# Kernel tuning notes

Measured on AMD Instinct MI355X. Metric: run time of the kernel, lower is better.

Reference implementation:

```python
import jax, jax.numpy as jnp
import numpy as np

EMB = 1024
HEADS = 16
HEAD_DIM = EMB // HEADS
DFF = 4 * EMB
EPS = 1e-5


def setup_inputs() -> dict:
    key = jax.random.key(0)
    ks = jax.random.split(key, 16)
    s = 0.02
    return {
        "x": jax.random.normal(ks[0], (4, 2048, EMB), dtype=jnp.float32),
        "Wq_w": jax.random.normal(ks[1], (EMB, EMB), jnp.float32) * s,
        "Wq_b": jnp.zeros((EMB,), jnp.float32),
        "Wk_w": jax.random.normal(ks[2], (EMB, EMB), jnp.float32) * s,
        "Wk_b": jnp.zeros((EMB,), jnp.float32),
        "Wv_w": jax.random.normal(ks[3], (EMB, EMB), jnp.float32) * s,
        "Wv_b": jnp.zeros((EMB,), jnp.float32),
        "Wo_w": jax.random.normal(ks[4], (EMB, EMB), jnp.float32) * s,
        "Wo_b": jnp.zeros((EMB,), jnp.float32),
        "l1_w": jax.random.normal(ks[5], (DFF, EMB), jnp.float32) * s,
        "l1_b": jnp.zeros((DFF,), jnp.float32),
        "l2_w": jax.random.normal(ks[6], (EMB, DFF), jnp.float32) * s,
        "l2_b": jnp.zeros((EMB,), jnp.float32),
        "n1_scale": jnp.ones((EMB,), jnp.float32),
        "n1_shift": jnp.zeros((EMB,), jnp.float32),
        "n2_scale": jnp.ones((EMB,), jnp.float32),
        "n2_shift": jnp.zeros((EMB,), jnp.float32),
    }


def _layernorm(x, scale, shift):
    # Faithful to the source: mean over last dim, but var over the WHOLE
    # tensor (torch.var with no dim), and divides by var (not std), eps added after.
    mean = jnp.mean(x, axis=-1, keepdims=True)
    var = jnp.var(x)  # scalar, correction=0
    x_norm = (x - mean) / var + EPS
    return x_norm * scale + shift


def _block_forward(x, Wq_w, Wq_b, Wk_w, Wk_b, Wv_w, Wv_b, Wo_w, Wo_b,
                   l1_w, l1_b, l2_w, l2_b, n1_scale, n1_shift, n2_scale, n2_shift):
    B, T, C = x.shape
    shortcut = x
    h = _layernorm(x, n1_scale, n1_shift)

    def proj(w, b):
        y = jnp.einsum('btc,oc->bto', h, w) + b
        return y.reshape(B, T, HEADS, HEAD_DIM).transpose(0, 2, 1, 3)  # bhtd

    q = proj(Wq_w, Wq_b)
    k = proj(Wk_w, Wk_b)
    v = proj(Wv_w, Wv_b)

    scores = jnp.einsum('bhtd,bhsd->bhts', q, k)
    causal = jnp.triu(jnp.ones((T, T), dtype=bool), 1)
    scores = jnp.where(causal, -jnp.inf, scores)
    weights = jax.nn.softmax(scores / jnp.sqrt(jnp.float32(HEAD_DIM)), axis=-1)
    ctx = jnp.einsum('bhts,bhsd->bhtd', weights, v)
    ctx = ctx.transpose(0, 2, 1, 3).reshape(B, T, C)
    attn_out = jnp.einsum('btc,oc->bto', ctx, Wo_w) + Wo_b

    x = attn_out + shortcut
    shortcut = x
    h = _layernorm(x, n2_scale, n2_shift)
    h = jnp.einsum('btc,fc->btf', h, l1_w) + l1_b
    h = jax.nn.gelu(h, approximate=False)
    h = jnp.einsum('btf,cf->btc', h, l2_w) + l2_b
    return h + shortcut


def reference(x, Wq_w, Wq_b, Wk_w, Wk_b, Wv_w, Wv_b, Wo_w, Wo_b,
              l1_w, l1_b, l2_w, l2_b, n1_scale, n1_shift, n2_scale, n2_shift):
    return _block_forward(x, Wq_w, Wq_b, Wk_w, Wk_b, Wv_w, Wv_b, Wo_w, Wo_b,
                          l1_w, l1_b, l2_w, l2_b, n1_scale, n1_shift, n2_scale, n2_shift)
```

## Files before the change

### kernel.cpp

```cpp
#include <hip/hip_runtime.h>
#include <cstdint>

#define EMB   1024
#define HEADS 16
#define HDIM  64
#define DFF   4096
#define TLEN  2048
#define BATCH 4
#define SEQB  8192
#define EPSLN 1e-5f

typedef __attribute__((ext_vector_type(8))) short bf16x8;
typedef __attribute__((ext_vector_type(4))) float f32x4;

#define MFMA16(a, b, c) __builtin_amdgcn_mfma_f32_16x16x32_bf16((a), (b), (c), 0, 0, 0)

__device__ __forceinline__ unsigned short f2bf(float f) {
  unsigned int u = __float_as_uint(f);
  u += 0x7fffu + ((u >> 16) & 1u);
  return (unsigned short)(u >> 16);
}

__device__ __forceinline__ float gelu_f(float x) {
  float x2 = x * x;
  float inner = x * (0.79788456f + 0.035677408f * x2);
  float t = exp2f(2.885390082f * inner);
  return x * t / (t + 1.0f);
}

__global__ __launch_bounds__(256) void cvt_bf16(const float* __restrict__ in,
                                                unsigned short* __restrict__ out, int n4) {
  int i = blockIdx.x * 256 + threadIdx.x;
  if (i >= n4) return;
  float4 v = ((const float4*)in)[i];
  ushort4 o;
  o.x = f2bf(v.x); o.y = f2bf(v.y); o.z = f2bf(v.z); o.w = f2bf(v.w);
  ((ushort4*)out)[i] = o;
}

__global__ __launch_bounds__(256) void pack3(const float* __restrict__ a,
                                             const float* __restrict__ b,
                                             const float* __restrict__ c,
                                             float* __restrict__ o) {
  int i = blockIdx.x * 256 + threadIdx.x;
  o[i] = i < 1024 ? a[i] : (i < 2048 ? b[i - 1024] : c[i - 2048]);
}

__global__ __launch_bounds__(256) void row_reduce(const float* __restrict__ X,
                                                  float* __restrict__ rs,
                                                  float* __restrict__ rq) {
  const int row = blockIdx.x;
  const int tid = threadIdx.x;
  float4 v = ((const float4*)(X + (long)row * EMB))[tid];
  float s = v.x + v.y + v.z + v.w;
  float q = v.x * v.x + v.y * v.y + v.z * v.z + v.w * v.w;
#pragma unroll
  for (int d = 1; d < 64; d <<= 1) { s += __shfl_xor(s, d); q += __shfl_xor(q, d); }
  __shared__ float ss[4], sq[4];
  const int wv = tid >> 6;
  if ((tid & 63) == 0) { ss[wv] = s; sq[wv] = q; }
  __syncthreads();
  if (tid == 0) {
    rs[row] = ss[0] + ss[1] + ss[2] + ss[3];
    rq[row] = sq[0] + sq[1] + sq[2] + sq[3];
  }
}

__global__ __launch_bounds__(256) void finalize_stats(const float* __restrict__ rs,
                                                      const float* __restrict__ rq,
                                                      float* __restrict__ stats) {
  const int tid = threadIdx.x;
  float s = 0.f, q = 0.f;
  for (int i = tid; i < SEQB; i += 256) { s += rs[i]; q += rq[i]; }
#pragma unroll
  for (int d = 1; d < 64; d <<= 1) { s += __shfl_xor(s, d); q += __shfl_xor(q, d); }
  __shared__ float ss[4], sq[4];
  const int wv = tid >> 6;
  if ((tid & 63) == 0) { ss[wv] = s; sq[wv] = q; }
  __syncthreads();
  if (tid == 0) {
    double n = (double)SEQB * (double)EMB;
    double mean = (double)(ss[0] + ss[1] + ss[2] + ss[3]) / n;
    double var = (double)(sq[0] + sq[1] + sq[2] + sq[3]) / n - mean * mean;
    stats[0] = (float)(1.0 / var);
  }
}

__global__ __launch_bounds__(256) void ln_apply(const float* __restrict__ X,
                                                const float* __restrict__ rs,
                                                const float* __restrict__ stats,
                                                const float* __restrict__ scale,
                                                const float* __restrict__ shift,
                                                unsigned short* __restrict__ H) {
  const long i = (long)blockIdx.x * 256 + threadIdx.x;
  const long idx = i * 4;
  const int row = (int)(idx >> 10);
  const int c = (int)(idx & 1023);
  const float mean = rs[row] * (1.0f / EMB);
  const float iv = stats[0];
  float4 x = ((const float4*)X)[i];
  float4 sc = *(const float4*)(scale + c);
  float4 sh = *(const float4*)(shift + c);
  ushort4 o;
  o.x = f2bf(((x.x - mean) * iv + EPSLN) * sc.x + sh.x);
  o.y = f2bf(((x.y - mean) * iv + EPSLN) * sc.y + sh.y);
  o.z = f2bf(((x.z - mean) * iv + EPSLN) * sc.z + sh.z);
  o.w = f2bf(((x.w - mean) * iv + EPSLN) * sc.w + sh.w);
  ((ushort4*)H)[i] = o;
}

#define STAGE_HALF(GSRC, LDST)                                                              \
  do {                                                                                      \
    _Pragma("unroll") for (int j_ = 0; j_ < 2; ++j_) {                                      \
      __builtin_amdgcn_global_load_lds(                                                     \
          (const __attribute__((address_space(1))) void*)((GSRC) +                          \
                                                          (long)(j_ * 128 + (tid >> 2)) * K), \
          (__attribute__((address_space(3))) void*)((LDST) + j_ * 4096 + tid * 8), 16, 0, 0); \
    }                                                                                       \
  } while (0)

template <int EPI>
__global__ __launch_bounds__(512, 2) void gemm8(const unsigned short* __restrict__ A,
                                                const unsigned short* __restrict__ W,
                                                const float* __restrict__ bias,
                                                const float* __restrict__ resid,
                                                void* __restrict__ Cout,
                                                unsigned short* __restrict__ kout,
                                                unsigned short* __restrict__ vout,
                                                int M, int N, int K) {
  __shared__ unsigned short lds[2][2][2][8192];
  const int tid = threadIdx.x;
  const int lane = tid & 63;
  const int wave = tid >> 6;
  const int wm = (wave >> 2) * 128, wn = (wave & 3) * 64;
  const int col = lane & 15, quad = lane >> 4;
  const int rq8 = (quad ^ ((col >> 1) & 3)) * 8;
  const int scol = ((tid & 3) ^ ((tid >> 3) & 3)) * 8;

  const int gx = (int)gridDim.x, gy = (int)gridDim.y;
  const int nwg = gx * gy;
  int bid = (int)blockIdx.y * gx + (int)blockIdx.x;
  if ((nwg & 7) == 0) bid = (bid & 7) * (nwg >> 3) + (bid >> 3);
  const long bm = (long)(bid / gx) * 256, bn = (long)(bid % gx) * 256;

  const unsigned short* Abase = A + bm * K;
  const unsigned short* Bbase = W + bn * K;

  f32x4 acc[8][4];
#pragma unroll
  for (int i = 0; i < 8; ++i)
#pragma unroll
    for (int j = 0; j < 4; ++j) acc[i][j] = (f32x4){0.f, 0.f, 0.f, 0.f};

  STAGE_HALF(Abase + scol, &lds[0][0][0][0]);
  STAGE_HALF(Bbase + scol, &lds[0][1][0][0]);
  STAGE_HALF(Abase + 32 + scol, &lds[0][0][1][0]);
  STAGE_HALF(Bbase + 32 + scol, &lds[0][1][1][0]);

  const int nk = K >> 6;
  for (int t = 0; t < nk; ++t) {
    const int c = t & 1;
    const bool pf = (t + 1) < nk;
    const long koff = (long)(t + 1) * 64;
    unsigned short* sAc = &lds[c][0][0][0];
    unsigned short* sBc = &lds[c][1][0][0];
    unsigned short* sAn = &lds[c ^ 1][0][0][0];
    unsigned short* sBn = &lds[c ^ 1][1][0][0];
    bf16x8 af[4], bfr[4];

    asm volatile("s_waitcnt vmcnt(4)" ::: "memory");
    __builtin_amdgcn_sched_barrier(0);
    __builtin_amdgcn_s_barrier();
    asm volatile("" ::: "memory");
    if (pf) STAGE_HALF(Abase + koff + scol, sAn);
#pragma unroll
    for (int nt = 0; nt < 4; ++nt) bfr[nt] = *(const bf16x8*)&sBc[(wn + nt * 16 + col) * 32 + rq8];
#pragma unroll
    for (int mt = 0; mt < 4; ++mt) af[mt] = *(const bf16x8*)&sAc[(wm + mt * 16 + col) * 32 + rq8];
    asm volatile("s_waitcnt lgkmcnt(0)" ::: "memory");
    __builtin_amdgcn_sched_barrier(0);
    __builtin_amdgcn_s_setprio(1);
#pragma unroll
    for (int mt = 0; mt < 4; ++mt)
#pragma unroll
      for (int nt = 0; nt < 4; ++nt) acc[mt][nt] = MFMA16(af[mt], bfr[nt], acc[mt][nt]);
    __builtin_amdgcn_s_setprio(0);

    __builtin_amdgcn_sched_barrier(0);
    __builtin_amdgcn_s_barrier();
    asm volatile("" ::: "memory");
    if (pf) STAGE_HALF(Bbase + koff + scol, sBn);
#pragma unroll
    for (int mt = 0; mt < 4; ++mt) af[mt] = *(const bf16x8*)&sAc[(wm + (mt + 4) * 16 + col) * 32 + rq8];
    asm volatile("s_waitcnt lgkmcnt(0)" ::: "memory");
    __builtin_amdgcn_sched_barrier(0);
    __builtin_amdgcn_s_setprio(1);
#pragma unroll
    for (int mt = 0; mt < 4; ++mt)
#pragma unroll
      for (int nt = 0; nt < 4; ++nt) acc[mt + 4][nt] = MFMA16(af[mt], bfr[nt], acc[mt + 4][nt]);
    __builtin_amdgcn_s_setprio(0);

    if (pf) asm volatile("s_waitcnt vmcnt(4)" ::: "memory");
    else    asm volatile("s_waitcnt vmcnt(0)" ::: "memory");
    __builtin_amdgcn_sched_barrier(0);
    __builtin_amdgcn_s_barrier();
    asm volatile("" ::: "memory");
    if (pf) STAGE_HALF(Abase + koff + 32 + scol, sAn + 8192);
#pragma unroll
    for (int nt = 0; nt < 4; ++nt) bfr[nt] = *(const bf16x8*)&sBc[8192 + (wn + nt * 16 + col) * 32 + rq8];
#pragma unroll
    for (int mt = 0; mt < 4; ++mt) af[mt] = *(const bf16x8*)&sAc[8192 + (wm + mt * 16 + col) * 32 + rq8];
    asm volatile("s_waitcnt lgkmcnt(0)" ::: "memory");
    __builtin_amdgcn_sched_barrier(0);
    __builtin_amdgcn_s_setprio(1);
#pragma unroll
    for (int mt = 0; mt < 4; ++mt)
#pragma unroll
      for (int nt = 0; nt < 4; ++nt) acc[mt][nt] = MFMA16(af[mt], bfr[nt], acc[mt][nt]);
    __builtin_amdgcn_s_setprio(0);

    __builtin_amdgcn_sched_barrier(0);
    __builtin_amdgcn_s_barrier();
    asm volatile("" ::: "memory");
    if (pf) STAGE_HALF(Bbase + koff + 32 + scol, sBn + 8192);
#pragma unroll
    for (int mt = 0; mt < 4; ++mt) af[mt] = *(const bf16x8*)&sAc[8192 + (wm + (mt + 4) * 16 + col) * 32 + rq8];
    asm volatile("s_waitcnt lgkmcnt(0)" ::: "memory");
    __builtin_amdgcn_sched_barrier(0);
    __builtin_amdgcn_s_setprio(1);
#pragma unroll
    for (int mt = 0; mt < 4; ++mt)
#pragma unroll
      for (int nt = 0; nt < 4; ++nt) acc[mt + 4][nt] = MFMA16(af[mt], bfr[nt], acc[mt + 4][nt]);
    __builtin_amdgcn_s_setprio(0);
  }

#pragma unroll
  for (int mt = 0; mt < 8; ++mt) {
    const long row0 = bm + wm + mt * 16 + quad * 4;
#pragma unroll
    for (int nt = 0; nt < 4; ++nt) {
      const long c = bn + wn + nt * 16 + col;
      const float bv = bias[c];
      if (EPI == 4) {
        const int seg = (int)(bn >> 10);
        if (seg == 2) {
          ushort4 o;
#pragma unroll
          for (int r = 0; r < 4; ++r) o[r] = f2bf(acc[mt][nt][r] + bv);
          const long bidx = row0 >> 11;
          const long t0 = row0 & 2047;
          *(ushort4*)(vout + (((bidx * 1024 + (c & 1023)) << 11) + t0)) = o;
        } else {
          unsigned short* dst = seg == 0 ? (unsigned short*)Cout : kout;
#pragma unroll
          for (int r = 0; r < 4; ++r)
            dst[(row0 + r) * 1024 + (c & 1023)] = f2bf(acc[mt][nt][r] + bv);
        }
      } else {
#pragma unroll
        for (int r = 0; r < 4; ++r) {
          const long row = row0 + r;
          float v = acc[mt][nt][r] + bv;
          if (EPI == 1) {
            ((float*)Cout)[row * N + c] = v + resid[row * N + c];
          } else {
            ((unsigned short*)Cout)[row * N + c] = f2bf(gelu_f(v));
          }
        }
      }
    }
  }
}

#define PSTR 136
__global__ __launch_bounds__(512, 4) void attn7(const unsigned short* __restrict__ Qb,
                                                const unsigned short* __restrict__ Kb,
                                                const unsigned short* __restrict__ vT,
                                                unsigned short* __restrict__ Ctx) {
  __shared__ unsigned short sK[128 * 64];
  __shared__ unsigned short sV[64 * 128];
  __shared__ unsigned short sP[8][16 * PSTR];
  const int bh = blockIdx.x;
  const int pair = blockIdx.y;
  const int b = bh >> 4, h = bh & 15;
  const int tid = threadIdx.x, lane = tid & 63, w = tid >> 6;
  const int col = lane & 15, quad = lane >> 4;
  const int cx = (col & 7) * 8;
  const long bbase = (long)b * TLEN;
  const long hoff = (long)h * HDIM;
  const unsigned short* vbase = vT + (((long)b * 16 + h) * HDIM << 11);
  const float sc2 = 0.125f * 1.44269504088896340736f;

  const int krow = tid >> 3;
  const int kcol = ((tid & 7) * 8) ^ ((krow & 7) * 8);
  const int vrow = tid >> 4;
  const int vcol = ((tid & 15) * 8) ^ ((vrow & 7) * 8);

  for (int phase = 0; phase < 2; ++phase) {
    const int qt = phase == 0 ? (15 - pair) : pair;

    bf16x8 qf[2];
    {
      const long t = (long)qt * 128 + w * 16 + col;
      const unsigned short* qp = Qb + (bbase + t) * EMB + hoff;
#pragma unroll
      for (int ks = 0; ks < 2; ++ks) qf[ks] = *(const bf16x8*)(qp + ks * 32 + quad * 8);
    }

    float li[4] = {0.f, 0.f, 0.f, 0.f};
    f32x4 o[4];
#pragma unroll
    for (int dt = 0; dt < 4; ++dt) o[dt] = (f32x4){0.f, 0.f, 0.f, 0.f};

    for (int kv = 0; kv <= qt; ++kv) {
      __syncthreads();
#pragma unroll
      for (int it = 0; it < 2; ++it) {
        const unsigned short* gk = Kb + (bbase + (long)kv * 128 + it * 64 + krow) * EMB + hoff + kcol;
        __builtin_amdgcn_global_load_lds((const __attribute__((address_space(1))) void*)gk,
                                         (__attribute__((address_space(3))) void*)&sK[it * 4096 + tid * 8],
                                         16, 0, 0);
        const unsigned short* gv = vbase + ((long)(it * 32 + vrow) << 11) + kv * 128 + vcol;
        __builtin_amdgcn_global_load_lds((const __attribute__((address_space(1))) void*)gv,
                                         (__attribute__((address_space(3))) void*)&sV[it * 4096 + tid * 8],
                                         16, 0, 0);
      }
      __syncthreads();

      f32x4 sa[8];
#pragma unroll
      for (int nt = 0; nt < 8; ++nt) sa[nt] = (f32x4){0.f, 0.f, 0.f, 0.f};
#pragma unroll
      for (int ks = 0; ks < 2; ++ks) {
        const int off = (ks * 32 + quad * 8) ^ cx;
#pragma unroll
        for (int nt = 0; nt < 8; ++nt) {
          bf16x8 kf = *(const bf16x8*)&sK[(nt * 16 + col) * 64 + off];
          sa[nt] = MFMA16(qf[ks], kf, sa[nt]);
        }
      }

      if (kv == qt) {
#pragma unroll
        for (int nt = 0; nt < 8; ++nt)
#pragma unroll
          for (int r = 0; r < 4; ++r) {
            const int trel = w * 16 + quad * 4 + r;
            const int srel = nt * 16 + col;
            if (srel > trel) sa[nt][r] = -INFINITY;
          }
      }

#pragma unroll
      for (int nt = 0; nt < 8; ++nt)
#pragma unroll
        for (int r = 0; r < 4; ++r) {
          const float p = exp2f(sa[nt][r] * sc2);
          li[r] += p;
          sP[w][(quad * 4 + r) * PSTR + nt * 16 + col] = f2bf(p);
        }

#pragma unroll
      for (int ks = 0; ks < 4; ++ks) {
        bf16x8 pa = *(const bf16x8*)&sP[w][col * PSTR + ks * 32 + quad * 8];
        const int voff = (ks * 32 + quad * 8) ^ cx;
#pragma unroll
        for (int dt = 0; dt < 4; ++dt) {
          bf16x8 vf = *(const bf16x8*)&sV[(dt * 16 + col) * 128 + voff];
          o[dt] = MFMA16(pa, vf, o[dt]);
        }
      }
    }

#pragma unroll
    for (int d = 1; d < 16; d <<= 1)
#pragma unroll
      for (int r = 0; r < 4; ++r) li[r] += __shfl_xor(li[r], d);
#pragma unroll
    for (int r = 0; r < 4; ++r) {
      const long t = (long)qt * 128 + w * 16 + quad * 4 + r;
      const float inv = 1.0f / li[r];
      unsigned short* cp = Ctx + (bbase + t) * EMB + hoff;
#pragma unroll
      for (int dt = 0; dt < 4; ++dt) cp[dt * 16 + col] = f2bf(o[dt][r] * inv);
    }
  }
}

extern "C" void kernel_launch(void* const* d_in, const int* in_sizes, int n_in,
                              void* d_out, int out_size, void* d_ws, size_t ws_size,
                              hipStream_t stream) {
  const float* x    = (const float*)d_in[0];
  const float* Wq_w = (const float*)d_in[1];
  const float* Wq_b = (const float*)d_in[2];
  const float* Wk_w = (const float*)d_in[3];
  const float* Wk_b = (const float*)d_in[4];
  const float* Wv_w = (const float*)d_in[5];
  const float* Wv_b = (const float*)d_in[6];
  const float* Wo_w = (const float*)d_in[7];
  const float* Wo_b = (const float*)d_in[8];
  const float* l1_w = (const float*)d_in[9];
  const float* l1_b = (const float*)d_in[10];
  const float* l2_w = (const float*)d_in[11];
  const float* l2_b = (const float*)d_in[12];
  const float* n1s  = (const float*)d_in[13];
  const float* n1h  = (const float*)d_in[14];
  const float* n2s  = (const float*)d_in[15];
  const float* n2h  = (const float*)d_in[16];

  char* ws = (char*)d_ws;
  const size_t MB = (size_t)1 << 20;
  unsigned short* wqkv = (unsigned short*)(ws + 0 * MB);
  unsigned short* wo = (unsigned short*)(ws + 6 * MB);
  unsigned short* l1 = (unsigned short*)(ws + 8 * MB);
  unsigned short* l2 = (unsigned short*)(ws + 16 * MB);
  unsigned short* hb = (unsigned short*)(ws + 24 * MB);
  unsigned short* qb = (unsigned short*)(ws + 40 * MB);
  unsigned short* kb = (unsigned short*)(ws + 56 * MB);
  unsigned short* vb = (unsigned short*)(ws + 72 * MB);
  unsigned short* cb = (unsigned short*)(ws + 88 * MB);
  unsigned short* gb = qb;
  float* x2 = (float*)(ws + 104 * MB);
  float* rs = (float*)(ws + 136 * MB);
  float* rq = (float*)(ws + 136 * MB + 64 * 1024);
  float* st = (float*)(ws + 136 * MB + 128 * 1024);
  float* bqkv = (float*)(ws + 136 * MB + 192 * 1024);

  cvt_bf16<<<1024, 256, 0, stream>>>(Wq_w, wqkv, EMB * EMB / 4);
  cvt_bf16<<<1024, 256, 0, stream>>>(Wk_w, wqkv + 1024 * 1024, EMB * EMB / 4);
  cvt_bf16<<<1024, 256, 0, stream>>>(Wv_w, wqkv + 2048 * 1024, EMB * EMB / 4);
  cvt_bf16<<<1024, 256, 0, stream>>>(Wo_w, wo, EMB * EMB / 4);
  cvt_bf16<<<4096, 256, 0, stream>>>(l1_w, l1, DFF * EMB / 4);
  cvt_bf16<<<4096, 256, 0, stream>>>(l2_w, l2, EMB * DFF / 4);
  pack3<<<12, 256, 0, stream>>>(Wq_b, Wk_b, Wv_b, bqkv);

  row_reduce<<<SEQB, 256, 0, stream>>>(x, rs, rq);
  finalize_stats<<<1, 256, 0, stream>>>(rs, rq, st);
  ln_apply<<<SEQB, 256, 0, stream>>>(x, rs, st, n1s, n1h, hb);

  dim3 g256(EMB / 256, SEQB / 256);
  gemm8<4><<<dim3(3 * EMB / 256, SEQB / 256), 512, 0, stream>>>(
      hb, wqkv, bqkv, nullptr, qb, kb, vb, SEQB, 3 * EMB, EMB);

  attn7<<<dim3(BATCH * HEADS, 8), 512, 0, stream>>>(qb, kb, vb, cb);

  gemm8<1><<<g256, 512, 0, stream>>>(cb, wo, Wo_b, x, (void*)x2, nullptr, nullptr, SEQB, EMB, EMB);

  row_reduce<<<SEQB, 256, 0, stream>>>(x2, rs, rq);
  finalize_stats<<<1, 256, 0, stream>>>(rs, rq, st);
  ln_apply<<<SEQB, 256, 0, stream>>>(x2, rs, st, n2s, n2h, hb);

  gemm8<2><<<dim3(DFF / 256, SEQB / 256), 512, 0, stream>>>(hb, l1, l1_b, nullptr, gb, nullptr, nullptr, SEQB, DFF, EMB);
  gemm8<1><<<g256, 512, 0, stream>>>(gb, l2, l2_b, x2, d_out, nullptr, nullptr, SEQB, EMB, DFF);
}
```

Before: 594.6 us.

## Restructure GEMM LDS pipeline to prefetch two k-steps ahead in place

Rewrites the GEMM main loop so global-to-LDS loads are issued up to two k-tiles ahead, reusing each half-buffer as soon as its fragments are read into registers. Barriers are placed after the LDS reads instead of before the staging, and a deeper prologue fills seven of the eight half-tiles. The goal is to hide more global memory latency behind MFMA work. The cost is more barriers per iteration and tighter vmcnt accounting, with a risk of WAR hazards if the barrier placement is subtly wrong.

```diff
diff --git a/kernel.cpp b/kernel.cpp
--- a/kernel.cpp
+++ b/kernel.cpp
@@ -120,7 +120,7 @@
   } while (0)
 
 template <int EPI>
-__global__ __launch_bounds__(512, 2) void gemm8(const unsigned short* __restrict__ A,
+__global__ __launch_bounds__(512, 2) void gemm9(const unsigned short* __restrict__ A,
                                                 const unsigned short* __restrict__ W,
                                                 const float* __restrict__ bias,
                                                 const float* __restrict__ resid,
@@ -152,31 +152,37 @@
 #pragma unroll
     for (int j = 0; j < 4; ++j) acc[i][j] = (f32x4){0.f, 0.f, 0.f, 0.f};
 
-  STAGE_HALF(Abase + scol, &lds[0][0][0][0]);
-  STAGE_HALF(Bbase + scol, &lds[0][1][0][0]);
+  const int nk = K >> 6;
+
+  STAGE_HALF(Bbase + scol,      &lds[0][1][0][0]);
+  STAGE_HALF(Abase + scol,      &lds[0][0][0][0]);
+  STAGE_HALF(Bbase + 32 + scol, &lds[0][1][1][0]);
   STAGE_HALF(Abase + 32 + scol, &lds[0][0][1][0]);
-  STAGE_HALF(Bbase + 32 + scol, &lds[0][1][1][0]);
-
-  const int nk = K >> 6;
+  STAGE_HALF(Bbase + 64 + scol, &lds[1][1][0][0]);
+  STAGE_HALF(Abase + 64 + scol, &lds[1][0][0][0]);
+  STAGE_HALF(Bbase + 96 + scol, &lds[1][1][1][0]);
+  if (nk > 2) asm volatile("s_waitcnt vmcnt(6)" ::: "memory");
+  else        asm volatile("s_waitcnt vmcnt(0)" ::: "memory");
+  __builtin_amdgcn_s_barrier();
+
   for (int t = 0; t < nk; ++t) {
     const int c = t & 1;
-    const bool pf = (t + 1) < nk;
-    const long koff = (long)(t + 1) * 64;
-    unsigned short* sAc = &lds[c][0][0][0];
-    unsigned short* sBc = &lds[c][1][0][0];
-    unsigned short* sAn = &lds[c ^ 1][0][0][0];
-    unsigned short* sBn = &lds[c ^ 1][1][0][0];
+    const bool pf1 = (t + 1) < nk;
+    const bool pf2 = (t + 2) < nk;
+    const long k1 = (long)(t + 1) * 64;
+    const long k2 = (long)(t + 2) * 64;
+    unsigned short* sA0 = &lds[c][0][0][0];
+    unsigned short* sA1 = &lds[c][0][1][0];
+    unsigned short* sB0 = &lds[c][1][0][0];
+    unsigned short* sB1 = &lds[c][1][1][0];
     bf16x8 af[4], bfr[4];
 
-    asm volatile("s_waitcnt vmcnt(4)" ::: "memory");
-    __builtin_amdgcn_sched_barrier(0);
-    __builtin_amdgcn_s_barrier();
-    asm volatile("" ::: "memory");
-    if (pf) STAGE_HALF(Abase + koff + scol, sAn);
-#pragma unroll
-    for (int nt = 0; nt < 4; ++nt) bfr[nt] = *(const bf16x8*)&sBc[(wn + nt * 16 + col) * 32 + rq8];
-#pragma unroll
-    for (int mt = 0; mt < 4; ++mt) af[mt] = *(const bf16x8*)&sAc[(wm + mt * 16 + col) * 32 + rq8];
+#pragma unroll
+    for (int nt = 0; nt < 4; ++nt) bfr[nt] = *(const bf16x8*)&sB0[(wn + nt * 16 + col) * 32 + rq8];
+#pragma unroll
+    for (int mt = 0; mt < 4; ++mt) af[mt] = *(const bf16x8*)&sA0[(wm + mt * 16 + col) * 32 + rq8];
+    if (pf1) STAGE_HALF(Abase + k1 + 32 + scol, &lds[c ^ 1][0][1][0]);
+    __builtin_amdgcn_s_barrier();
     asm volatile("s_waitcnt lgkmcnt(0)" ::: "memory");
     __builtin_amdgcn_sched_barrier(0);
     __builtin_amdgcn_s_setprio(1);
@@ -185,13 +191,12 @@
 #pragma unroll
       for (int nt = 0; nt < 4; ++nt) acc[mt][nt] = MFMA16(af[mt], bfr[nt], acc[mt][nt]);
     __builtin_amdgcn_s_setprio(0);
-
-    __builtin_amdgcn_sched_barrier(0);
-    __builtin_amdgcn_s_barrier();
-    asm volatile("" ::: "memory");
-    if (pf) STAGE_HALF(Bbase + koff + scol, sBn);
-#pragma unroll
-    for (int mt = 0; mt < 4; ++mt) af[mt] = *(const bf16x8*)&sAc[(wm + (mt + 4) * 16 + col) * 32 + rq8];
+    __builtin_amdgcn_s_barrier();
+
+#pragma unroll
+    for (int mt = 0; mt < 4; ++mt) af[mt] = *(const bf16x8*)&sA0[(wm + (mt + 4) * 16 + col) * 32 + rq8];
+    if (pf2) STAGE_HALF(Bbase + k2 + scol, &lds[c][1][0][0]);
+    __builtin_amdgcn_s_barrier();
     asm volatile("s_waitcnt lgkmcnt(0)" ::: "memory");
     __builtin_amdgcn_sched_barrier(0);
     __builtin_amdgcn_s_setprio(1);
@@ -200,17 +205,14 @@
 #pragma unroll
       for (int nt = 0; nt < 4; ++nt) acc[mt + 4][nt] = MFMA16(af[mt], bfr[nt], acc[mt + 4][nt]);
     __builtin_amdgcn_s_setprio(0);
-
-    if (pf) asm volatile("s_waitcnt vmcnt(4)" ::: "memory");
-    else    asm volatile("s_waitcnt vmcnt(0)" ::: "memory");
-    __builtin_amdgcn_sched_barrier(0);
-    __builtin_amdgcn_s_barrier();
-    asm volatile("" ::: "memory");
-    if (pf) STAGE_HALF(Abase + koff + 32 + scol, sAn + 8192);
-#pragma unroll
-    for (int nt = 0; nt < 4; ++nt) bfr[nt] = *(const bf16x8*)&sBc[8192 + (wn + nt * 16 + col) * 32 + rq8];
-#pragma unroll
-    for (int mt = 0; mt < 4; ++mt) af[mt] = *(const bf16x8*)&sAc[8192 + (wm + mt * 16 + col) * 32 + rq8];
+    __builtin_amdgcn_s_barrier();
+
+#pragma unroll
+    for (int nt = 0; nt < 4; ++nt) bfr[nt] = *(const bf16x8*)&sB1[(wn + nt * 16 + col) * 32 + rq8];
+#pragma unroll
+    for (int mt = 0; mt < 4; ++mt) af[mt] = *(const bf16x8*)&sA1[(wm + mt * 16 + col) * 32 + rq8];
+    if (pf2) STAGE_HALF(Abase + k2 + scol, &lds[c][0][0][0]);
+    __builtin_amdgcn_s_barrier();
     asm volatile("s_waitcnt lgkmcnt(0)" ::: "memory");
     __builtin_amdgcn_sched_barrier(0);
     __builtin_amdgcn_s_setprio(1);
@@ -219,13 +221,12 @@
 #pragma unroll
       for (int nt = 0; nt < 4; ++nt) acc[mt][nt] = MFMA16(af[mt], bfr[nt], acc[mt][nt]);
     __builtin_amdgcn_s_setprio(0);
-
-    __builtin_amdgcn_sched_barrier(0);
-    __builtin_amdgcn_s_barrier();
-    asm volatile("" ::: "memory");
-    if (pf) STAGE_HALF(Bbase + koff + 32 + scol, sBn + 8192);
-#pragma unroll
-    for (int mt = 0; mt < 4; ++mt) af[mt] = *(const bf16x8*)&sAc[8192 + (wm + (mt + 4) * 16 + col) * 32 + rq8];
+    __builtin_amdgcn_s_barrier();
+
+#pragma unroll
+    for (int mt = 0; mt < 4; ++mt) af[mt] = *(const bf16x8*)&sA1[(wm + (mt + 4) * 16 + col) * 32 + rq8];
+    if (pf2) STAGE_HALF(Bbase + k2 + 32 + scol, &lds[c][1][1][0]);
+    __builtin_amdgcn_s_barrier();
     asm volatile("s_waitcnt lgkmcnt(0)" ::: "memory");
     __builtin_amdgcn_sched_barrier(0);
     __builtin_amdgcn_s_setprio(1);
@@ -234,6 +235,11 @@
 #pragma unroll
       for (int nt = 0; nt < 4; ++nt) acc[mt + 4][nt] = MFMA16(af[mt], bfr[nt], acc[mt + 4][nt]);
     __builtin_amdgcn_s_setprio(0);
+    if (pf1) {
+      if (pf2) asm volatile("s_waitcnt vmcnt(6)" ::: "memory");
+      else     asm volatile("s_waitcnt vmcnt(0)" ::: "memory");
+    }
+    __builtin_amdgcn_s_barrier();
   }
 
 #pragma unroll
@@ -441,17 +447,17 @@
   ln_apply<<<SEQB, 256, 0, stream>>>(x, rs, st, n1s, n1h, hb);
 
   dim3 g256(EMB / 256, SEQB / 256);
-  gemm8<4><<<dim3(3 * EMB / 256, SEQB / 256), 512, 0, stream>>>(
+  gemm9<4><<<dim3(3 * EMB / 256, SEQB / 256), 512, 0, stream>>>(
       hb, wqkv, bqkv, nullptr, qb, kb, vb, SEQB, 3 * EMB, EMB);
 
   attn7<<<dim3(BATCH * HEADS, 8), 512, 0, stream>>>(qb, kb, vb, cb);
 
-  gemm8<1><<<g256, 512, 0, stream>>>(cb, wo, Wo_b, x, (void*)x2, nullptr, nullptr, SEQB, EMB, EMB);
+  gemm9<1><<<g256, 512, 0, stream>>>(cb, wo, Wo_b, x, (void*)x2, nullptr, nullptr, SEQB, EMB, EMB);
 
   row_reduce<<<SEQB, 256, 0, stream>>>(x2, rs, rq);
   finalize_stats<<<1, 256, 0, stream>>>(rs, rq, st);
   ln_apply<<<SEQB, 256, 0, stream>>>(x2, rs, st, n2s, n2h, hb);
 
-  gemm8<2><<<dim3(DFF / 256, SEQB / 256), 512, 0, stream>>>(hb, l1, l1_b, nullptr, gb, nullptr, nullptr, SEQB, DFF, EMB);
-  gemm8<1><<<g256, 512, 0, stream>>>(gb, l2, l2_b, x2, d_out, nullptr, nullptr, SEQB, EMB, DFF);
-}
+  gemm9<2><<<dim3(DFF / 256, SEQB / 256), 512, 0, stream>>>(hb, l1, l1_b, nullptr, gb, nullptr, nullptr, SEQB, DFF, EMB);
+  gemm9<1><<<g256, 512, 0, stream>>>(gb, l2, l2_b, x2, d_out, nullptr, nullptr, SEQB, EMB, DFF);
+}
```

Result: no change. 584.6 us (-1.7%).
